# Kernel tuning notes

Hardware: AMD Instinct MI355X
Metric: run time of the kernel (lower is better)

The kernel has to match this reference:

```python
import jax, jax.numpy as jnp
import numpy as np

N = 50000; E = 1600000; F = 128; H = 128; C = 40; G = 4
GRID = jnp.linspace(-2.0, 2.0, G)          # FastKAN default grid [-2, 2]
DENOM = 4.0 / (G - 1)                      # (grid_max - grid_min) / (num_grids - 1)
EPS = 1e-5
DIMS = [(F, H), (H, H), (F + 2 * H, C)]    # conv0, conv1, conv_out (skip concat)


def setup_inputs() -> dict:
    key = jax.random.key(0)
    ks = iter(jax.random.split(key, 64))
    inp = {}
    inp["x"] = jax.random.normal(next(ks), (N, F), jnp.float32)
    inp["edge_index"] = jax.random.randint(next(ks), (2, E), 0, N)
    for i, (di, do) in enumerate(DIMS):
        inp[f"c{i}_ln_g"] = jnp.ones((di,), jnp.float32)
        inp[f"c{i}_ln_b"] = jnp.zeros((di,), jnp.float32)
        inp[f"c{i}_sw"] = jax.random.normal(next(ks), (do, di * G), jnp.float32) * 0.1
        inp[f"c{i}_sb"] = jnp.zeros((do,), jnp.float32)
        inp[f"c{i}_bw"] = jax.random.normal(next(ks), (do, di), jnp.float32) * (1.0 / np.sqrt(di))
        inp[f"c{i}_bb"] = jnp.zeros((do,), jnp.float32)
        inp[f"c{i}_bias"] = jnp.zeros((do,), jnp.float32)   # GCNConv output bias
    inp["bn_g"] = jnp.ones((H,), jnp.float32)
    inp["bn_b"] = jnp.zeros((H,), jnp.float32)
    return inp


def _fkan(h, lg, lb, sw, sb, bw, bb):
    # FastKANLayer: LayerNorm -> RBF basis -> spline linear, plus SiLU base branch
    mu = h.mean(-1, keepdims=True)
    var = jnp.mean(jnp.square(h - mu), -1, keepdims=True)
    hn = (h - mu) * jax.lax.rsqrt(var + EPS) * lg + lb
    basis = jnp.exp(-jnp.square((hn[..., None] - GRID) / DENOM))  # [N, d, G]
    basis = basis.reshape(h.shape[0], -1)                          # [N, d*G]
    return basis @ sw.T + sb + jax.nn.silu(h) @ bw.T + bb


def _forward(x, edge_index, params, bn_g, bn_b):
    # gcn_norm with self-loops, symmetric normalization
    row = jnp.concatenate([edge_index[0], jnp.arange(N)])
    col = jnp.concatenate([edge_index[1], jnp.arange(N)])
    deg = jax.ops.segment_sum(jnp.ones_like(row, jnp.float32), col, num_segments=N)
    dis = jnp.where(deg > 0, jax.lax.rsqrt(jnp.maximum(deg, 1e-12)), 0.0)
    norm = dis[row] * dis[col]

    def conv(h, p):
        hw = _fkan(h, *p[:6])  # lin = FKANLayer applied before propagate
        return jax.ops.segment_sum(norm[:, None] * hw[row], col, num_segments=N) + p[6]

    def bn(h):  # BatchNorm1d, training-mode batch stats (biased var); dropout p=0
        mu = h.mean(0)
        var = jnp.mean(jnp.square(h - mu), 0)
        return (h - mu) * jax.lax.rsqrt(var + EPS) * bn_g + bn_b

    skips = [x]
    h = x
    for p in params[:-1]:
        h = bn(conv(h, p))
        skips.append(h)
    h = jnp.concatenate(skips, axis=1)  # skip=True
    return conv(h, params[-1])


def reference(x, edge_index, c0_ln_g, c0_ln_b, c0_sw, c0_sb, c0_bw, c0_bb, c0_bias,
              c1_ln_g, c1_ln_b, c1_sw, c1_sb, c1_bw, c1_bb, c1_bias,
              c2_ln_g, c2_ln_b, c2_sw, c2_sb, c2_bw, c2_bb, c2_bias, bn_g, bn_b):
    params = [
        (c0_ln_g, c0_ln_b, c0_sw, c0_sb, c0_bw, c0_bb, c0_bias),
        (c1_ln_g, c1_ln_b, c1_sw, c1_sb, c1_bw, c1_bb, c1_bias),
        (c2_ln_g, c2_ln_b, c2_sw, c2_sb, c2_bw, c2_bb, c2_bias),
    ]
    return _forward(x, edge_index, params, bn_g, bn_b)
```

## Files before the change

### kernel.cpp

```cpp
#include <hip/hip_runtime.h>
#include <math.h>

constexpr int NN = 50000;
constexpr int NE = 1600000;
constexpr float LN_EPS = 1e-5f;

constexpr int NBKT  = 8;
constexpr int SPAN  = NN / NBKT;
constexpr int CHUNK = 8192;
constexpr int NB1   = (NE + CHUNK - 1) / CHUNK;
constexpr int NSB   = (NN + 255) / 256;

typedef __attribute__((ext_vector_type(8))) short short8;
typedef __attribute__((ext_vector_type(4))) float f32x4;

__device__ __forceinline__ short f2bf(float f)
{
    unsigned u = __builtin_bit_cast(unsigned, f);
    u += 0x7fffu + ((u >> 16) & 1u);
    return (short)(u >> 16);
}

__device__ __forceinline__ float2 bf2x2(unsigned p)
{
    float2 r;
    r.x = __builtin_bit_cast(float, p << 16);
    r.y = __builtin_bit_cast(float, p & 0xffff0000u);
    return r;
}

__global__ __launch_bounds__(256) void csr_hist(const int* __restrict__ col,
                                                int* __restrict__ degi,
                                                int* __restrict__ histo)
{
    __shared__ int hcnt[NBKT];
    const int tid = threadIdx.x;
    if (tid < NBKT) hcnt[tid] = 0;
    __syncthreads();
    const int e0 = blockIdx.x * CHUNK;
    const int e1 = min(e0 + CHUNK, NE);
    for (int e = e0 + tid; e < e1; e += 256) {
        int c = col[e];
        atomicAdd(&degi[c], 1);
        atomicAdd(&hcnt[(unsigned)c / (unsigned)SPAN], 1);
    }
    __syncthreads();
    if (tid < NBKT) histo[tid * NB1 + blockIdx.x] = hcnt[tid];
}

__global__ __launch_bounds__(256) void csr_scan2(int* __restrict__ histo)
{
    constexpr int M = NBKT * NB1;
    constexpr int T = (M + 255) / 256;
    __shared__ int part[256];
    const int t = threadIdx.x;
    int v[T];
    int s = 0;
    #pragma unroll
    for (int j = 0; j < T; ++j) {
        int i = t * T + j;
        v[j] = (i < M) ? histo[i] : 0;
        s += v[j];
    }
    part[t] = s;
    __syncthreads();
    for (int d = 1; d < 256; d <<= 1) {
        int add = (t >= d) ? part[t - d] : 0;
        __syncthreads();
        part[t] += add;
        __syncthreads();
    }
    int run = part[t] - s;
    #pragma unroll
    for (int j = 0; j < T; ++j) {
        int i = t * T + j;
        if (i < M) { histo[i] = run; run += v[j]; }
    }
}

__global__ __launch_bounds__(256) void csr_part(const int* __restrict__ ei,
                                                const int* __restrict__ histo,
                                                uint2* __restrict__ staging)
{
    __shared__ int lcur[NBKT];
    const int tid = threadIdx.x;
    if (tid < NBKT) lcur[tid] = histo[tid * NB1 + blockIdx.x];
    __syncthreads();
    const int e0 = blockIdx.x * CHUNK;
    const int e1 = min(e0 + CHUNK, NE);
    for (int e = e0 + tid; e < e1; e += 256) {
        int r = ei[e];
        int c = ei[NE + e];
        int slot = atomicAdd(&lcur[(unsigned)c / (unsigned)SPAN], 1);
        staging[slot] = make_uint2((unsigned)r, (unsigned)c);
    }
}

template<int PB2>
__global__ __launch_bounds__(256) void csr_scatter(const uint2* __restrict__ staging,
                                                   const int* __restrict__ off,
                                                   int* __restrict__ cur,
                                                   int* __restrict__ rows)
{
    const int b   = blockIdx.x & (NBKT - 1);
    const int blk = blockIdx.x >> 3;
    const int base = off[b * SPAN];
    const int end  = off[(b + 1) * SPAN];
    for (int i = base + blk * 256 + threadIdx.x; i < end; i += PB2 * 256) {
        uint2 e = staging[i];
        int p = off[e.y] + atomicAdd(&cur[e.y], 1);
        rows[p] = (int)e.x;
    }
}

__global__ void dis_kernel(const int* __restrict__ degi, float* __restrict__ dis)
{
    int i = blockIdx.x * 256 + threadIdx.x;
    if (i < NN) dis[i] = rsqrtf((float)degi[i] + 1.0f);
}

__global__ __launch_bounds__(256) void scan_p1(const int* __restrict__ deg,
                                               int* __restrict__ off,
                                               int* __restrict__ partials)
{
    __shared__ int sh[256];
    const int t = threadIdx.x;
    const int i = blockIdx.x * 256 + t;
    int v = (i < NN) ? deg[i] : 0;
    sh[t] = v;
    __syncthreads();
    for (int d = 1; d < 256; d <<= 1) {
        int add = (t >= d) ? sh[t - d] : 0;
        __syncthreads();
        sh[t] += add;
        __syncthreads();
    }
    if (i < NN) off[i] = sh[t] - v;
    if (t == 255) partials[blockIdx.x] = sh[255];
}

__global__ __launch_bounds__(256) void scan_p2(int* __restrict__ partials)
{
    __shared__ int sh[256];
    const int t = threadIdx.x;
    int v = (t < NSB) ? partials[t] : 0;
    sh[t] = v;
    __syncthreads();
    for (int d = 1; d < 256; d <<= 1) {
        int add = (t >= d) ? sh[t - d] : 0;
        __syncthreads();
        sh[t] += add;
        __syncthreads();
    }
    if (t < NSB) partials[t] = sh[t] - v;
    if (t == 255) partials[NSB] = sh[255];
}

__global__ __launch_bounds__(256) void scan_p3(int* __restrict__ off,
                                               const int* __restrict__ partials)
{
    const int i = blockIdx.x * 256 + threadIdx.x;
    if (i < NN) off[i] += partials[blockIdx.x];
    if (i == 0) off[NN] = partials[NSB];
}

__global__ void pack_frag(const float* __restrict__ sw, const float* __restrict__ bw,
                          short* __restrict__ wtf, int D, int OT, int DO, int total)
{
    int idx = blockIdx.x * 256 + threadIdx.x;
    if (idx >= total) return;
    int j8   = idx & 7;
    int lane = (idx >> 3) & 63;
    int rest = idx >> 9;
    int ot = rest % OT, kk = rest / OT;
    int g4 = lane >> 4;
    int s  = kk * 8 + j8;
    int f  = g4 * (D / 4) + s / 5;
    int g5 = s % 5;
    int o  = ot * 16 + (lane & 15);
    float val = 0.f;
    if (o < DO) val = (g5 < 4) ? sw[o * D * 4 + f * 4 + g5] : bw[o * D + f];
    wtf[idx] = f2bf(val);
}

__global__ void bn_id(float2* __restrict__ bnp)
{
    bnp[threadIdx.x] = make_float2(1.0f, 0.0f);
}

__global__ void bn_final(const float* __restrict__ stats, const float* __restrict__ g,
                         const float* __restrict__ b, float2* __restrict__ dst)
{
    int c = threadIdx.x;
    float mu  = stats[c] * (1.0f / NN);
    float var = stats[c + 128] * (1.0f / NN) - mu * mu;
    float rs  = rsqrtf(var + LN_EPS);
    float sc  = rs * g[c];
    dst[c] = make_float2(sc, b[c] - mu * sc);
}

template<int D, int DO, int OT, int KKC, int NODES, int WPE, bool RAWLDS, bool BN>
__global__ __launch_bounds__(NODES * 4, WPE) void fkan_reg(
    const float* __restrict__ s0, const float* __restrict__ s1, const float* __restrict__ s2,
    const float2* __restrict__ bnp,
    const float* __restrict__ ln_g, const float* __restrict__ ln_b,
    const short* __restrict__ wtf, const float* __restrict__ sb, const float* __restrict__ bb,
    short* __restrict__ out)
{
    constexpr int BW   = D / 4;
    constexpr int GBS  = BW + 1;
    constexpr int RS   = 4 * GBS + 1;
    constexpr int PPC  = KKC / 5;
    constexpr int NV   = RAWLDS ? 1 : (BW / 4);
    __shared__ unsigned pkL[NODES * RS];

    const int tid = threadIdx.x;
    const int anode = tid >> 2, q = tid & 3;
    const int gnode = blockIdx.x * NODES + anode;
    const int snode = (gnode < NN) ? gnode : (NN - 1);
    unsigned* prow = &pkL[anode * RS + q * GBS];

    float mu, rstd;
    float4 va[NV];
    {
        float sum = 0.f, sq = 0.f;
        #pragma unroll
        for (int i4 = 0; i4 < BW / 4; ++i4) {
            int f = q * BW + i4 * 4;
            const float* src = (D == 128) ? s0 : ((f < 128) ? s0 : (f < 256) ? s1 : s2);
            float4 v = *(const float4*)&src[snode * 128 + (f & 127)];
            if constexpr (BN) {
                float4 ba = *(const float4*)&bnp[f];
                float4 bc = *(const float4*)&bnp[f + 2];
                v.x = fmaf(v.x, ba.x, ba.y);
                v.y = fmaf(v.y, ba.z, ba.w);
                v.z = fmaf(v.z, bc.x, bc.y);
                v.w = fmaf(v.w, bc.z, bc.w);
            }
            if constexpr (RAWLDS) {
                prow[i4 * 4 + 0] = __builtin_bit_cast(unsigned, v.x);
                prow[i4 * 4 + 1] = __builtin_bit_cast(unsigned, v.y);
                prow[i4 * 4 + 2] = __builtin_bit_cast(unsigned, v.z);
                prow[i4 * 4 + 3] = __builtin_bit_cast(unsigned, v.w);
            } else {
                va[i4] = v;
            }
            sum += (v.x + v.y) + (v.z + v.w);
            sq  += (v.x * v.x + v.y * v.y) + (v.z * v.z + v.w * v.w);
        }
        sum += __shfl_xor(sum, 1); sum += __shfl_xor(sum, 2);
        sq  += __shfl_xor(sq, 1);  sq  += __shfl_xor(sq, 2);
        mu   = sum * (1.0f / D);
        rstd = rsqrtf(sq * (1.0f / D) - mu * mu + LN_EPS);
    }

    #pragma unroll
    for (int i4 = 0; i4 < BW / 4; ++i4) {
        int f = q * BW + i4 * 4;
        float4 v;
        if constexpr (RAWLDS) {
            v.x = __builtin_bit_cast(float, prow[i4 * 4 + 0]);
            v.y = __builtin_bit_cast(float, prow[i4 * 4 + 1]);
            v.z = __builtin_bit_cast(float, prow[i4 * 4 + 2]);
            v.w = __builtin_bit_cast(float, prow[i4 * 4 + 3]);
        } else {
            v = va[i4];
        }
        float4 lg = *(const float4*)&ln_g[f];
        float4 lb = *(const float4*)&ln_b[f];
        float hn[4], sl[4];
        hn[0] = (v.x - mu) * rstd * lg.x + lb.x;
        hn[1] = (v.y - mu) * rstd * lg.y + lb.y;
        hn[2] = (v.z - mu) * rstd * lg.z + lb.z;
        hn[3] = (v.w - mu) * rstd * lg.w + lb.w;
        sl[0] = v.x / (1.0f + __expf(-v.x));
        sl[1] = v.y / (1.0f + __expf(-v.y));
        sl[2] = v.z / (1.0f + __expf(-v.z));
        sl[3] = v.w / (1.0f + __expf(-v.w));
        #pragma unroll
        for (int k = 0; k < 4; ++k)
            prow[i4 * 4 + k] = ((unsigned)(unsigned short)f2bf(hn[k]) << 16)
                             | ((unsigned)(unsigned short)f2bf(sl[k]) & 0xffffu);
    }
    __syncthreads();

    const int wv = tid >> 6, lane = tid & 63;
    const int m = lane & 15, g4 = lane >> 4;
    const unsigned* pkb = &pkL[(wv * 16 + m) * RS + g4 * GBS];

    f32x4 acc[OT];
    #pragma unroll
    for (int ot = 0; ot < OT; ++ot) acc[ot] = f32x4{0.f, 0.f, 0.f, 0.f};

    union AU { unsigned u[4]; short8 s; };

    for (int pl = 0; pl < PPC; ++pl) {
        const unsigned* pp = pkb + pl * 8;
        const short* bp = wtf + (pl * 5) * OT * 512 + lane * 8;
        #pragma unroll
        for (int c = 0; c < 5; ++c) {
            constexpr int FL0[5] = {0, 1, 3, 4, 6};
            constexpr int NF[5]  = {2, 3, 2, 3, 2};
            unsigned p[3];
            float h75[3];
            #pragma unroll
            for (int i = 0; i < 3; ++i) {
                if (i < NF[c]) {
                    p[i]   = pp[FL0[c] + i];
                    h75[i] = __builtin_bit_cast(float, p[i] & 0xffff0000u) * 0.75f;
                }
            }
            AU a;
            #pragma unroll
            for (int i = 0; i < 4; ++i) {
                unsigned v2[2];
                #pragma unroll
                for (int h = 0; h < 2; ++h) {
                    int sl = c * 8 + 2 * i + h;
                    int fl = sl / 5 - FL0[c];
                    int g  = sl % 5;
                    if (g == 4) {
                        v2[h] = p[fl] & 0xffffu;
                    } else {
                        float t = h75[fl] + (1.5f - (float)g);
                        float e = __expf(-t * t);
                        v2[h] = (unsigned)(unsigned short)f2bf(e);
                    }
                }
                a.u[i] = (v2[0] & 0xffffu) | (v2[1] << 16);
            }
            #pragma unroll
            for (int ot = 0; ot < OT; ++ot) {
                short8 b = *(const short8*)(bp + (c * OT + ot) * 512);
                acc[ot] = __builtin_amdgcn_mfma_f32_16x16x32_bf16(a.s, b, acc[ot], 0, 0, 0);
            }
        }
    }

    const int nrow0 = blockIdx.x * NODES + wv * 16 + g4 * 4;
    #pragma unroll
    for (int ot = 0; ot < OT; ++ot) {
        int o = ot * 16 + m;
        if (o < DO) {
            float cb = sb[o] + bb[o];
            #pragma unroll
            for (int r = 0; r < 4; ++r) {
                int nr = nrow0 + r;
                if (nr < NN) out[nr * DO + o] = f2bf(acc[ot][r] + cb);
            }
        }
    }
}

template<int DO>
__global__ __launch_bounds__(64) void agg_gather_bf16(
    const int* __restrict__ off, const int* __restrict__ rows,
    const float* __restrict__ dis, const short* __restrict__ hwb,
    const float* __restrict__ bias, float* __restrict__ out)
{
    constexpr int ACT = DO / 2;
    const int n   = blockIdx.x;
    const int tid = threadIdx.x;
    __shared__ int   srow[64];
    __shared__ float swgt[64];

    const int e0 = off[n], e1 = off[n + 1];
    const float dn = dis[n];
    float ax = 0.f, ay = 0.f;
    if (tid < ACT) {
        unsigned p = *(const unsigned*)&hwb[n * DO + 2 * tid];
        float2 v = bf2x2(p);
        ax = dn * dn * v.x + bias[2 * tid];
        ay = dn * dn * v.y + bias[2 * tid + 1];
    }

    for (int t0 = e0; t0 < e1; t0 += 64) {
        const int nt = min(64, e1 - t0);
        if (tid < nt) {
            int r = rows[t0 + tid];
            srow[tid] = r;
            swgt[tid] = dn * dis[r];
        }
        __syncthreads();
        if (tid < ACT) {
            #pragma unroll 4
            for (int j = 0; j < nt; ++j) {
                unsigned p = *(const unsigned*)&hwb[srow[j] * DO + 2 * tid];
                float2 v = bf2x2(p);
                float w = swgt[j];
                ax += w * v.x;
                ay += w * v.y;
            }
        }
        __syncthreads();
    }
    if (tid < ACT) {
        out[n * DO + 2 * tid]     = ax;
        out[n * DO + 2 * tid + 1] = ay;
    }
}

__global__ void bn_stats(const float* __restrict__ h, float* __restrict__ stats)
{
    __shared__ float s1[256], s2[256];
    int c = threadIdx.x & 127;
    int half = threadIdx.x >> 7;
    float sum = 0.f, sq = 0.f;
    for (int n = blockIdx.x * 2 + half; n < NN; n += 512) {
        float v = h[n * 128 + c];
        sum += v; sq += v * v;
    }
    s1[threadIdx.x] = sum; s2[threadIdx.x] = sq;
    __syncthreads();
    if (half == 0) {
        s1[c] += s1[c + 128]; s2[c] += s2[c + 128];
        atomicAdd(&stats[c],        s1[c]);
        atomicAdd(&stats[c + 128],  s2[c]);
    }
}

extern "C" void kernel_launch(void* const* d_in, const int* in_sizes, int n_in,
                              void* d_out, int out_size, void* d_ws, size_t ws_size,
                              hipStream_t stream)
{
    auto F = [&](int i) { return (const float*)d_in[i]; };
    const float* x  = F(0);
    const int*   ei = (const int*)d_in[1];
    const float* bn_g = F(23);
    const float* bn_b = F(24);

    short*  wtf0 = (short*)d_ws;
    short*  wtf1 = wtf0 + 81920;
    short*  wtf2 = wtf1 + 81920;
    short*  hwb  = wtf2 + 92160;
    float*  dis  = (float*)(hwb + 6400000);
    float2* bnp  = (float2*)(dis + 50000);
    float*  h1   = (float*)(bnp + 384);
    float*  h2   = h1 + 6400000;
    float*  stats = h2 + 6400000;
    int*    degi = (int*)(stats + 256);
    int*    off  = degi + 50000;
    int*    cur  = off + 50001;
    int*    rows = cur + 50000;
    int*    histo = rows + NE;
    int*    partials = histo + NBKT * NB1;
    uint2*  staging = (uint2*)h1;
    float*  outf = (float*)d_out;

    (void)hipMemsetAsync(degi, 0, 50000 * sizeof(int), stream);
    (void)hipMemsetAsync(cur,  0, 50000 * sizeof(int), stream);
    csr_hist<<<NB1, 256, 0, stream>>>(ei + NE, degi, histo);
    dis_kernel<<<(NN + 255) / 256, 256, 0, stream>>>(degi, dis);
    scan_p1<<<NSB, 256, 0, stream>>>(degi, off, partials);
    scan_p2<<<1, 256, 0, stream>>>(partials);
    scan_p3<<<NSB, 256, 0, stream>>>(off, partials);
    csr_scan2<<<1, 256, 0, stream>>>(histo);
    csr_part<<<NB1, 256, 0, stream>>>(ei, histo, staging);
    csr_scatter<128><<<128 * NBKT, 256, 0, stream>>>(staging, off, cur, rows);

    pack_frag<<<(81920 + 255) / 256, 256, 0, stream>>>(F(4),  F(6),  wtf0, 128, 8, 128, 81920);
    pack_frag<<<(81920 + 255) / 256, 256, 0, stream>>>(F(11), F(13), wtf1, 128, 8, 128, 81920);
    pack_frag<<<(92160 + 255) / 256, 256, 0, stream>>>(F(18), F(20), wtf2, 384, 3, 40,  92160);
    bn_id<<<1, 128, 0, stream>>>(bnp);

    const int gridN64 = (NN + 63) / 64;
    const int gridN16 = (NN + 15) / 16;

    fkan_reg<128, 128, 8, 20, 64, 4, false, false><<<gridN64, 256, 0, stream>>>(x, nullptr, nullptr,
        nullptr, F(2), F(3), wtf0, F(5), F(7), hwb);
    agg_gather_bf16<128><<<NN, 64, 0, stream>>>(off, rows, dis, hwb, F(8), h1);
    (void)hipMemsetAsync(stats, 0, 256 * sizeof(float), stream);
    bn_stats<<<256, 256, 0, stream>>>(h1, stats);
    bn_final<<<1, 128, 0, stream>>>(stats, bn_g, bn_b, bnp + 128);

    fkan_reg<128, 128, 8, 20, 64, 4, false, true><<<gridN64, 256, 0, stream>>>(h1, nullptr, nullptr,
        bnp + 128, F(9), F(10), wtf1, F(12), F(14), hwb);
    agg_gather_bf16<128><<<NN, 64, 0, stream>>>(off, rows, dis, hwb, F(15), h2);
    (void)hipMemsetAsync(stats, 0, 256 * sizeof(float), stream);
    bn_stats<<<256, 256, 0, stream>>>(h2, stats);
    bn_final<<<1, 128, 0, stream>>>(stats, bn_g, bn_b, bnp + 256);

    fkan_reg<384, 40, 3, 60, 16, 2, true, true><<<gridN16, 64, 0, stream>>>(x, h1, h2,
        bnp, F(16), F(17), wtf2, F(19), F(21), hwb);
    agg_gather_bf16<40><<<NN, 64, 0, stream>>>(off, rows, dis, hwb, F(22), outf);
}
```

Measured before the change: 580.9 us.

## Split gather aggregation into channel slices with edge-parallel lanes per block

```diff
diff --git a/kernel.cpp b/kernel.cpp
--- a/kernel.cpp
+++ b/kernel.cpp
@@ -352,6 +352,60 @@
     }
 }
 
+template<int DO, int NS>
+__global__ __launch_bounds__(64) void agg_gather_sl(
+    const int* __restrict__ off, const int* __restrict__ rows,
+    const float* __restrict__ dis, const short* __restrict__ hwb,
+    const float* __restrict__ bias, float* __restrict__ out)
+{
+    constexpr int CPS = DO / NS;
+    const int slice = blockIdx.x & (NS - 1);
+    const int n     = blockIdx.x / NS;
+    const int tid = threadIdx.x;
+    const int c = tid & 7;
+    const int g = tid >> 3;
+    __shared__ int   srow[64];
+    __shared__ float swgt[64];
+
+    const int e0 = off[n], e1 = off[n + 1];
+    const float dn = dis[n];
+    const int ch0 = slice * CPS + 2 * c;
+    float ax = 0.f, ay = 0.f;
+    if (g == 0) {
+        unsigned p = *(const unsigned*)&hwb[n * DO + ch0];
+        float2 v = bf2x2(p);
+        ax = dn * dn * v.x + bias[ch0];
+        ay = dn * dn * v.y + bias[ch0 + 1];
+    }
+
+    for (int t0 = e0; t0 < e1; t0 += 64) {
+        const int nt = min(64, e1 - t0);
+        if (tid < nt) {
+            int r = rows[t0 + tid];
+            srow[tid] = r;
+            swgt[tid] = dn * dis[r];
+        }
+        __syncthreads();
+        for (int j = g; j < nt; j += 8) {
+            unsigned p = *(const unsigned*)&hwb[srow[j] * DO + ch0];
+            float2 v = bf2x2(p);
+            float w = swgt[j];
+            ax += w * v.x;
+            ay += w * v.y;
+        }
+        __syncthreads();
+    }
+    #pragma unroll
+    for (int mk = 8; mk < 64; mk <<= 1) {
+        ax += __shfl_xor(ax, mk);
+        ay += __shfl_xor(ay, mk);
+    }
+    if (g == 0) {
+        out[n * DO + ch0]     = ax;
+        out[n * DO + ch0 + 1] = ay;
+    }
+}
+
 template<int DO>
 __global__ __launch_bounds__(64) void agg_gather_bf16(
     const int* __restrict__ off, const int* __restrict__ rows,
@@ -468,14 +522,14 @@
 
     fkan_reg<128, 128, 8, 20, 64, 4, false, false><<<gridN64, 256, 0, stream>>>(x, nullptr, nullptr,
         nullptr, F(2), F(3), wtf0, F(5), F(7), hwb);
-    agg_gather_bf16<128><<<NN, 64, 0, stream>>>(off, rows, dis, hwb, F(8), h1);
+    agg_gather_sl<128, 8><<<NN * 8, 64, 0, stream>>>(off, rows, dis, hwb, F(8), h1);
     (void)hipMemsetAsync(stats, 0, 256 * sizeof(float), stream);
     bn_stats<<<256, 256, 0, stream>>>(h1, stats);
     bn_final<<<1, 128, 0, stream>>>(stats, bn_g, bn_b, bnp + 128);
 
     fkan_reg<128, 128, 8, 20, 64, 4, false, true><<<gridN64, 256, 0, stream>>>(h1, nullptr, nullptr,
         bnp + 128, F(9), F(10), wtf1, F(12), F(14), hwb);
-    agg_gather_bf16<128><<<NN, 64, 0, stream>>>(off, rows, dis, hwb, F(15), h2);
+    agg_gather_sl<128, 8><<<NN * 8, 64, 0, stream>>>(off, rows, dis, hwb, F(15), h2);
     (void)hipMemsetAsync(stats, 0, 256 * sizeof(float), stream);
     bn_stats<<<256, 256, 0, stream>>>(h2, stats);
     bn_final<<<1, 128, 0, stream>>>(stats, bn_g, bn_b, bnp + 256);
```

Result: slower. 825.5 us (+42.1%).

## Build MFMA A-fragments directly in registers for 128-wide FastKAN layers

Applied to the files above, without the earlier changes.

```diff
diff --git a/kernel.cpp b/kernel.cpp
--- a/kernel.cpp
+++ b/kernel.cpp
@@ -197,6 +197,119 @@
     float rs  = rsqrtf(var + LN_EPS);
     float sc  = rs * g[c];
     dst[c] = make_float2(sc, b[c] - mu * sc);
+}
+
+template<int DO, int OT, int KKC, bool BN>
+__global__ __launch_bounds__(256, 4) void fkan_rd(
+    const float* __restrict__ s0, const float2* __restrict__ bnp,
+    const float* __restrict__ ln_g, const float* __restrict__ ln_b,
+    const short* __restrict__ wtf, const float* __restrict__ sb, const float* __restrict__ bb,
+    short* __restrict__ out)
+{
+    const int tid  = threadIdx.x;
+    const int wv   = tid >> 6, lane = tid & 63;
+    const int m    = lane & 15, q = lane >> 4;
+    const int gnode = blockIdx.x * 64 + wv * 16 + m;
+    const int snode = (gnode < NN) ? gnode : (NN - 1);
+
+    float4 v[8];
+    float sum = 0.f, sq = 0.f;
+    #pragma unroll
+    for (int i = 0; i < 8; ++i) {
+        int f = q * 32 + i * 4;
+        float4 t = *(const float4*)&s0[snode * 128 + f];
+        if constexpr (BN) {
+            float4 ba = *(const float4*)&bnp[f];
+            float4 bc = *(const float4*)&bnp[f + 2];
+            t.x = fmaf(t.x, ba.x, ba.y);
+            t.y = fmaf(t.y, ba.z, ba.w);
+            t.z = fmaf(t.z, bc.x, bc.y);
+            t.w = fmaf(t.w, bc.z, bc.w);
+        }
+        v[i] = t;
+        sum += (t.x + t.y) + (t.z + t.w);
+        sq  += (t.x * t.x + t.y * t.y) + (t.z * t.z + t.w * t.w);
+    }
+    sum += __shfl_xor(sum, 16); sum += __shfl_xor(sum, 32);
+    sq  += __shfl_xor(sq, 16);  sq  += __shfl_xor(sq, 32);
+    const float mu   = sum * (1.0f / 128.0f);
+    const float rstd = rsqrtf(sq * (1.0f / 128.0f) - mu * mu + LN_EPS);
+
+    f32x4 acc[OT];
+    #pragma unroll
+    for (int ot = 0; ot < OT; ++ot) acc[ot] = f32x4{0.f, 0.f, 0.f, 0.f};
+
+    union AU { unsigned u[4]; short8 s; };
+
+    #pragma unroll
+    for (int pl = 0; pl < KKC / 5; ++pl) {
+        float hn[8], slv[8];
+        {
+            float4 lg0 = *(const float4*)&ln_g[q * 32 + pl * 8];
+            float4 lg1 = *(const float4*)&ln_g[q * 32 + pl * 8 + 4];
+            float4 lb0 = *(const float4*)&ln_b[q * 32 + pl * 8];
+            float4 lb1 = *(const float4*)&ln_b[q * 32 + pl * 8 + 4];
+            float4 va = v[pl * 2], vb = v[pl * 2 + 1];
+            hn[0] = (va.x - mu) * rstd * lg0.x + lb0.x;
+            hn[1] = (va.y - mu) * rstd * lg0.y + lb0.y;
+            hn[2] = (va.z - mu) * rstd * lg0.z + lb0.z;
+            hn[3] = (va.w - mu) * rstd * lg0.w + lb0.w;
+            hn[4] = (vb.x - mu) * rstd * lg1.x + lb1.x;
+            hn[5] = (vb.y - mu) * rstd * lg1.y + lb1.y;
+            hn[6] = (vb.z - mu) * rstd * lg1.z + lb1.z;
+            hn[7] = (vb.w - mu) * rstd * lg1.w + lb1.w;
+            slv[0] = va.x / (1.0f + __expf(-va.x));
+            slv[1] = va.y / (1.0f + __expf(-va.y));
+            slv[2] = va.z / (1.0f + __expf(-va.z));
+            slv[3] = va.w / (1.0f + __expf(-va.w));
+            slv[4] = vb.x / (1.0f + __expf(-vb.x));
+            slv[5] = vb.y / (1.0f + __expf(-vb.y));
+            slv[6] = vb.z / (1.0f + __expf(-vb.z));
+            slv[7] = vb.w / (1.0f + __expf(-vb.w));
+        }
+        const short* bp = wtf + (pl * 5) * OT * 512 + lane * 8;
+        #pragma unroll
+        for (int c = 0; c < 5; ++c) {
+            AU a;
+            #pragma unroll
+            for (int i = 0; i < 4; ++i) {
+                unsigned v2[2];
+                #pragma unroll
+                for (int h = 0; h < 2; ++h) {
+                    int s  = c * 8 + 2 * i + h;
+                    int fl = s / 5;
+                    int g  = s % 5;
+                    if (g == 4) {
+                        v2[h] = (unsigned)(unsigned short)f2bf(slv[fl]);
+                    } else {
+                        float t = hn[fl] * 0.75f + (1.5f - (float)g);
+                        float e = __expf(-t * t);
+                        v2[h] = (unsigned)(unsigned short)f2bf(e);
+                    }
+                }
+                a.u[i] = (v2[0] & 0xffffu) | (v2[1] << 16);
+            }
+            #pragma unroll
+            for (int ot = 0; ot < OT; ++ot) {
+                short8 b = *(const short8*)(bp + (c * OT + ot) * 512);
+                acc[ot] = __builtin_amdgcn_mfma_f32_16x16x32_bf16(a.s, b, acc[ot], 0, 0, 0);
+            }
+        }
+    }
+
+    const int nrow0 = blockIdx.x * 64 + wv * 16 + q * 4;
+    #pragma unroll
+    for (int ot = 0; ot < OT; ++ot) {
+        int o = ot * 16 + m;
+        if (o < DO) {
+            float cb = sb[o] + bb[o];
+            #pragma unroll
+            for (int r = 0; r < 4; ++r) {
+                int nr = nrow0 + r;
+                if (nr < NN) out[nr * DO + o] = f2bf(acc[ot][r] + cb);
+            }
+        }
+    }
 }
 
 template<int D, int DO, int OT, int KKC, int NODES, int WPE, bool RAWLDS, bool BN>
@@ -466,14 +579,14 @@
     const int gridN64 = (NN + 63) / 64;
     const int gridN16 = (NN + 15) / 16;
 
-    fkan_reg<128, 128, 8, 20, 64, 4, false, false><<<gridN64, 256, 0, stream>>>(x, nullptr, nullptr,
+    fkan_rd<128, 8, 20, false><<<gridN64, 256, 0, stream>>>(x,
         nullptr, F(2), F(3), wtf0, F(5), F(7), hwb);
     agg_gather_bf16<128><<<NN, 64, 0, stream>>>(off, rows, dis, hwb, F(8), h1);
     (void)hipMemsetAsync(stats, 0, 256 * sizeof(float), stream);
     bn_stats<<<256, 256, 0, stream>>>(h1, stats);
     bn_final<<<1, 128, 0, stream>>>(stats, bn_g, bn_b, bnp + 128);
 
-    fkan_reg<128, 128, 8, 20, 64, 4, false, true><<<gridN64, 256, 0, stream>>>(h1, nullptr, nullptr,
+    fkan_rd<128, 8, 20, true><<<gridN64, 256, 0, stream>>>(h1,
         bnp + 128, F(9), F(10), wtf1, F(12), F(14), hwb);
     agg_gather_bf16<128><<<NN, 64, 0, stream>>>(off, rows, dis, hwb, F(15), h2);
     (void)hipMemsetAsync(stats, 0, 256 * sizeof(float), stream);
```

Measured after the change: 540.1 us. 7.0% less time.
